# Kernel tuning notes

Measured on AMD Instinct MI355X. Metric: run time of the kernel, lower is better.

## Reference

```python
import jax, jax.numpy as jnp
import numpy as np

BN_EPS = 1e-5

def _batchnorm(x, gamma, beta):
    # torch BatchNorm1d in training mode: batch mean, biased variance
    mean = jnp.mean(x, axis=0)
    var = jnp.mean(jnp.square(x - mean), axis=0)
    return (x - mean) * jax.lax.rsqrt(var + BN_EPS) * gamma + beta

def setup_inputs() -> dict:
    key = jax.random.key(0)
    ks = jax.random.split(key, 6)
    N, E, D_atom, D_nbr = 50000, 1600000, 64, 64
    d_in, d_out = 2 * D_atom + D_nbr, 2 * D_atom  # 192, 128
    return {
        "atom_in_fea": jax.random.normal(ks[0], (N, D_atom), dtype=jnp.float32),
        "nbr_fea": jax.random.normal(ks[1], (E, D_nbr), dtype=jnp.float32),
        "edge_src": jax.random.randint(ks[2], (E,), 0, N),
        "edge_dst": jax.random.randint(ks[3], (E,), 0, N),
        "W": jax.random.normal(ks[4], (d_in, d_out), dtype=jnp.float32) * (1.0 / np.sqrt(d_in)),
        "b": jax.random.normal(ks[5], (d_out,), dtype=jnp.float32) * 0.01,
        "bn1_gamma": jnp.ones((d_out,), dtype=jnp.float32),
        "bn1_beta": jnp.zeros((d_out,), dtype=jnp.float32),
        "bn2_gamma": jnp.ones((D_atom,), dtype=jnp.float32),
        "bn2_beta": jnp.zeros((D_atom,), dtype=jnp.float32),
    }

def reference(atom_in_fea, nbr_fea, edge_src, edge_dst, W, b,
              bn1_gamma, bn1_beta, bn2_gamma, bn2_beta):
    N, D = atom_in_fea.shape
    # gather endpoints, concat with edge features: [E, 2D + D_nbr]
    total_fea = jnp.concatenate(
        [atom_in_fea[edge_src], atom_in_fea[edge_dst], nbr_fea], axis=1)
    total_fea = _batchnorm(total_fea @ W + b, bn1_gamma, bn1_beta)
    filter_fea, core_fea = jnp.split(total_fea, 2, axis=1)
    nbr_msg = jax.nn.sigmoid(filter_fea) * jax.nn.softplus(core_fea)  # [E, D]
    # scatter-add messages to destination atoms
    atom_update = jax.ops.segment_sum(nbr_msg, edge_dst, num_segments=N)
    atom_update = _batchnorm(atom_update, bn2_gamma, bn2_beta)
    return jax.nn.softplus(atom_in_fea + atom_update)
```

## Files before the change

### kernel.cpp

```cpp
#include <hip/hip_runtime.h>
#include <hip/hip_bf16.h>

typedef __attribute__((ext_vector_type(8))) short short8;
typedef __attribute__((ext_vector_type(4))) float floatx4;

__device__ __forceinline__ float bits2f(unsigned short u) {
    union { unsigned int i; float f; } v; v.i = ((unsigned int)u) << 16; return v.f;
}
__device__ __forceinline__ unsigned short f2bb(float x) {
    union { float f; unsigned int i; } v; v.f = x;
    unsigned int r = v.i + 0x7FFFu + ((v.i >> 16) & 1u);
    return (unsigned short)(r >> 16);
}
__device__ __forceinline__ float ldf(const void* base, long i, int fp32) {
    return fp32 ? ((const float*)base)[i] : bits2f(((const unsigned short*)base)[i]);
}
__device__ __forceinline__ short8 loadRow8(const void* base, long off, int fp32) {
    short8 r;
    if (!fp32) {
        r = *(const short8*)((const unsigned short*)base + off);
    } else {
        const float* f = (const float*)base + off;
        #pragma unroll
        for (int j = 0; j < 8; ++j) r[j] = (short)f2bb(f[j]);
    }
    return r;
}
__device__ __forceinline__ float lclamp(float z) {
    return fminf(fmaxf(z, -1e4f), 1e4f);
}

__global__ void k_probe(const unsigned short* __restrict__ Wb, int* __restrict__ flag) {
    int t = threadIdx.x;
    unsigned short u = Wb[t * 2];
    unsigned e = (u >> 7) & 0xFF;
    int in = (e >= 0x60 && e <= 0x8F) ? 1 : 0;
    unsigned long long m = __ballot(in);
    if (t == 0) flag[0] = (__popcll(m) < 32) ? 1 : 0;
}

__global__ __launch_bounds__(256) void k_atom_proj(
    const void* __restrict__ atom,
    const void* __restrict__ Wv,
    const void* __restrict__ bv,
    __hip_bfloat16* __restrict__ P, int N, const int* __restrict__ flagp)
{
    const int fp32 = *flagp;
    const int t = threadIdx.x;
    const int wave = t >> 6, lane = t & 63;
    const int half = wave & 1;
    const int pairInBlk = wave >> 1;
    const int n0 = lane & 15, kq = lane >> 4;

    short8 bf[8][2];
    #pragma unroll
    for (int tt = 0; tt < 8; ++tt)
        #pragma unroll
        for (int h = 0; h < 2; ++h)
            #pragma unroll
            for (int jj = 0; jj < 8; ++jj) {
                int k = half*64 + h*32 + kq*8 + jj;
                bf[tt][h][jj] = (short)f2bb(ldf(Wv, (long)k*128 + tt*16 + n0, fp32));
            }
    float bias[8];
    #pragma unroll
    for (int tt = 0; tt < 8; ++tt)
        bias[tt] = half ? 0.f : ldf(bv, tt*16 + n0, fp32);

    const long nGroups = ((long)N + 15) / 16;
    for (long g = (long)blockIdx.x*2 + pairInBlk; g < nGroups; g += (long)gridDim.x*2) {
        long a0 = g * 16;
        long am = a0 + n0;
        short8 a_lo = {}, a_hi = {};
        if (am < N) {
            a_lo = loadRow8(atom, am*64 + kq*8, fp32);
            a_hi = loadRow8(atom, am*64 + 32 + kq*8, fp32);
        }
        #pragma unroll
        for (int tt = 0; tt < 8; ++tt) {
            floatx4 c = {0.f, 0.f, 0.f, 0.f};
            c = __builtin_amdgcn_mfma_f32_16x16x32_bf16(a_lo, bf[tt][0], c, 0, 0, 0);
            c = __builtin_amdgcn_mfma_f32_16x16x32_bf16(a_hi, bf[tt][1], c, 0, 0, 0);
            #pragma unroll
            for (int r = 0; r < 4; ++r) {
                long a = a0 + kq*4 + r;
                if (a < N)
                    P[a*256 + half*128 + tt*16 + n0] =
                        __float2bfloat16(lclamp(c[r] + bias[tt]));
            }
        }
    }
}

template<int PHASE>
__global__ __launch_bounds__(256) void k_edge(
    const void* __restrict__ nbr,
    const int* __restrict__ esrc,
    const int* __restrict__ edst,
    const void* __restrict__ Wv,
    const unsigned short* __restrict__ Pb,
    const float* __restrict__ coef,
    float* __restrict__ outAcc,
    long E, const int* __restrict__ flagp)
{
    __shared__ float s_sum[128], s_ss[128];
    const int fp32 = *flagp;
    const int t = threadIdx.x;
    const int wave = t >> 6, lane = t & 63;
    const int n0 = lane & 15, kq = lane >> 4;

    short8 bf[8][2];
    #pragma unroll
    for (int tt = 0; tt < 8; ++tt)
        #pragma unroll
        for (int h = 0; h < 2; ++h)
            #pragma unroll
            for (int jj = 0; jj < 8; ++jj) {
                int k = 128 + h*32 + kq*8 + jj;
                bf[tt][h][jj] = (short)f2bb(ldf(Wv, (long)k*128 + tt*16 + n0, fp32));
            }

    float sc[8], sh[8];
    if (PHASE == 1) {
        #pragma unroll
        for (int tt = 0; tt < 8; ++tt) {
            sc[tt] = coef[tt*16 + n0];
            sh[tt] = coef[128 + tt*16 + n0];
        }
    }
    float lsum[8], lss[8];
    if (PHASE == 0) {
        if (t < 128) { s_sum[t] = 0.f; s_ss[t] = 0.f; }
        #pragma unroll
        for (int tt = 0; tt < 8; ++tt) { lsum[tt] = 0.f; lss[tt] = 0.f; }
    }

    const long nGroups = (E + 15) / 16;
    for (long g = (long)blockIdx.x*4 + wave; g < nGroups; g += (long)gridDim.x*4) {
        long e0 = g * 16;
        long ea = e0 + n0;
        short8 a_lo = {}, a_hi = {};
        if (ea < E) {
            a_lo = loadRow8(nbr, ea*64 + kq*8, fp32);
            a_hi = loadRow8(nbr, ea*64 + 32 + kq*8, fp32);
        }
        floatx4 acc[8];
        #pragma unroll
        for (int tt = 0; tt < 8; ++tt) {
            floatx4 c = {0.f, 0.f, 0.f, 0.f};
            c = __builtin_amdgcn_mfma_f32_16x16x32_bf16(a_lo, bf[tt][0], c, 0, 0, 0);
            c = __builtin_amdgcn_mfma_f32_16x16x32_bf16(a_hi, bf[tt][1], c, 0, 0, 0);
            acc[tt] = c;
        }
        int sE[4], dE[4];
        #pragma unroll
        for (int r = 0; r < 4; ++r) {
            long er = e0 + kq*4 + r;
            sE[r] = (er < E) ? esrc[er] : 0;
            dE[r] = (er < E) ? edst[er] : 0;
        }
        if (PHASE == 0) {
            #pragma unroll
            for (int tt = 0; tt < 8; ++tt) {
                int n = tt*16 + n0;
                #pragma unroll
                for (int r = 0; r < 4; ++r) {
                    long er = e0 + kq*4 + r;
                    if (er < E) {
                        float z = lclamp(acc[tt][r]
                                + bits2f(Pb[(long)sE[r]*256 + n])
                                + bits2f(Pb[(long)dE[r]*256 + 128 + n]));
                        lsum[tt] += z; lss[tt] += z*z;
                    }
                }
            }
        } else {
            float zh[8][4];
            #pragma unroll
            for (int tt = 0; tt < 8; ++tt) {
                int n = tt*16 + n0;
                #pragma unroll
                for (int r = 0; r < 4; ++r) {
                    float z = lclamp(acc[tt][r]
                            + bits2f(Pb[(long)sE[r]*256 + n])
                            + bits2f(Pb[(long)dE[r]*256 + 128 + n]));
                    zh[tt][r] = z * sc[tt] + sh[tt];
                }
            }
            #pragma unroll
            for (int tt = 0; tt < 4; ++tt) {
                #pragma unroll
                for (int r = 0; r < 4; ++r) {
                    long er = e0 + kq*4 + r;
                    if (er < E) {
                        float f = zh[tt][r], c = zh[tt+4][r];
                        float sig = 1.f / (1.f + __expf(-f));
                        float sp  = fmaxf(c, 0.f) + log1pf(__expf(-fabsf(c)));
                        atomicAdd(outAcc + (long)dE[r]*64 + tt*16 + n0, sig * sp);
                    }
                }
            }
        }
    }
    if (PHASE == 0) {
        __syncthreads();
        #pragma unroll
        for (int tt = 0; tt < 8; ++tt) {
            atomicAdd(&s_sum[tt*16 + n0], lsum[tt]);
            atomicAdd(&s_ss[tt*16 + n0], lss[tt]);
        }
        __syncthreads();
        if (t < 128) {
            atomicAdd(&outAcc[t], s_sum[t]);
            atomicAdd(&outAcc[128 + t], s_ss[t]);
        }
    }
}

__global__ void k_fin1(const float* __restrict__ stats,
                       const void* __restrict__ gamma,
                       const void* __restrict__ beta,
                       float* __restrict__ coef, float invE,
                       const int* __restrict__ flagp)
{
    const int fp32 = *flagp;
    int t = threadIdx.x;
    float mean = stats[t] * invE;
    float var  = fmaxf(stats[128 + t] * invE - mean * mean, 0.f);
    float sc = ldf(gamma, t, fp32) * rsqrtf(var + 1e-5f);
    coef[t] = sc;
    coef[128 + t] = ldf(beta, t, fp32) - mean * sc;
}

__global__ void k_au_stats(const float* __restrict__ au, float* __restrict__ stats, int N)
{
    __shared__ float s_red[256];
    int t = threadIdx.x;
    int j = t & 63, r = t >> 6;
    float lsum = 0.f, lss = 0.f;
    for (int base = blockIdx.x * 4; base < N; base += gridDim.x * 4) {
        int a = base + r;
        if (a < N) { float v = au[(long)a*64 + j]; lsum += v; lss += v*v; }
    }
    s_red[t] = lsum; __syncthreads();
    if (t < 64) atomicAdd(&stats[j], s_red[j] + s_red[j+64] + s_red[j+128] + s_red[j+192]);
    __syncthreads();
    s_red[t] = lss; __syncthreads();
    if (t < 64) atomicAdd(&stats[64+j], s_red[j] + s_red[j+64] + s_red[j+128] + s_red[j+192]);
}

__global__ void k_fin2(const float* __restrict__ stats,
                       const void* __restrict__ gamma,
                       const void* __restrict__ beta,
                       float* __restrict__ coef, float invN,
                       const int* __restrict__ flagp)
{
    const int fp32 = *flagp;
    int t = threadIdx.x;
    float mean = stats[t] * invN;
    float var  = fmaxf(stats[64 + t] * invN - mean * mean, 0.f);
    float sc = ldf(gamma, t, fp32) * rsqrtf(var + 1e-5f);
    coef[t] = sc;
    coef[64 + t] = ldf(beta, t, fp32) - mean * sc;
}

__global__ void k_out(const void* __restrict__ atom,
                      const float* __restrict__ au,
                      const float* __restrict__ coef2,
                      void* __restrict__ out, long total,
                      const int* __restrict__ flagp)
{
    const int fp32 = *flagp;
    long i = (long)blockIdx.x * blockDim.x + threadIdx.x;
    if (i >= total) return;
    int j = (int)(i & 63);
    float x = lclamp(ldf(atom, i, fp32) + au[i] * coef2[j] + coef2[64 + j]);
    float sp = fmaxf(x, 0.f) + log1pf(__expf(-fabsf(x)));
    if (fp32) ((float*)out)[i] = sp;
    else      ((__hip_bfloat16*)out)[i] = __float2bfloat16(sp);
}

extern "C" void kernel_launch(void* const* d_in, const int* in_sizes, int n_in,
                              void* d_out, int out_size, void* d_ws, size_t ws_size,
                              hipStream_t stream)
{
    const void* atom = d_in[0];
    const void* nbr  = d_in[1];
    const int* esrc = (const int*)d_in[2];
    const int* edst = (const int*)d_in[3];
    const void* Wv  = d_in[4];
    const void* bv  = d_in[5];
    const void* g1  = d_in[6];
    const void* be1 = d_in[7];
    const void* g2  = d_in[8];
    const void* be2 = d_in[9];

    const int  N = in_sizes[0] / 64;
    const long E = (long)in_sizes[1] / 64;

    char* w = (char*)d_ws;
    __hip_bfloat16* P = (__hip_bfloat16*)w;  w += (size_t)N * 256 * sizeof(__hip_bfloat16);
    float* au     = (float*)w;               w += (size_t)N * 64 * sizeof(float);
    float* stats1 = (float*)w;               w += 256 * sizeof(float);
    float* stats2 = (float*)w;               w += 128 * sizeof(float);
    float* coef1  = (float*)w;               w += 256 * sizeof(float);
    float* coef2  = (float*)w;               w += 128 * sizeof(float);
    int* flagp    = (int*)w;

    hipMemsetAsync(au, 0, (size_t)N * 64 * sizeof(float), stream);
    hipMemsetAsync(stats1, 0, 384 * sizeof(float), stream);

    k_probe<<<1, 64, 0, stream>>>((const unsigned short*)Wv, flagp);
    k_atom_proj<<<1024, 256, 0, stream>>>(atom, Wv, bv, P, N, flagp);
    k_edge<0><<<2048, 256, 0, stream>>>(nbr, esrc, edst, Wv,
                                        (const unsigned short*)P, nullptr, stats1, E, flagp);
    k_fin1<<<1, 128, 0, stream>>>(stats1, g1, be1, coef1, 1.0f / (float)E, flagp);
    k_edge<1><<<2048, 256, 0, stream>>>(nbr, esrc, edst, Wv,
                                        (const unsigned short*)P, coef1, au, E, flagp);
    k_au_stats<<<1024, 256, 0, stream>>>(au, stats2, N);
    k_fin2<<<1, 64, 0, stream>>>(stats2, g2, be2, coef2, 1.0f / (float)N, flagp);
    long total = (long)N * 64;
    k_out<<<(int)((total + 255) / 256), 256, 0, stream>>>(atom, au, coef2,
                                                          d_out, total, flagp);
}
```

Measured before the change: 1.716 ms.

## Materialize edge pre-activations in bf16 to avoid recomputing GEMM and gathers

```diff
diff --git a/kernel.cpp b/kernel.cpp
--- a/kernel.cpp
+++ b/kernel.cpp
@@ -3,6 +3,7 @@
 
 typedef __attribute__((ext_vector_type(8))) short short8;
 typedef __attribute__((ext_vector_type(4))) float floatx4;
+typedef __attribute__((ext_vector_type(4))) unsigned short us4;
 
 __device__ __forceinline__ float bits2f(unsigned short u) {
     union { unsigned int i; float f; } v; v.i = ((unsigned int)u) << 16; return v.f;
@@ -40,10 +41,9 @@
 }
 
 __global__ __launch_bounds__(256) void k_atom_proj(
-    const void* __restrict__ atom,
-    const void* __restrict__ Wv,
-    const void* __restrict__ bv,
-    __hip_bfloat16* __restrict__ P, int N, const int* __restrict__ flagp)
+    const void* __restrict__ atom, const void* __restrict__ Wv,
+    const void* __restrict__ bv, __hip_bfloat16* __restrict__ P,
+    int N, const int* __restrict__ flagp)
 {
     const int fp32 = *flagp;
     const int t = threadIdx.x;
@@ -92,15 +92,14 @@
     }
 }
 
-template<int PHASE>
-__global__ __launch_bounds__(256) void k_edge(
+__global__ __launch_bounds__(256) void k_edge_gemm(
     const void* __restrict__ nbr,
     const int* __restrict__ esrc,
     const int* __restrict__ edst,
     const void* __restrict__ Wv,
     const unsigned short* __restrict__ Pb,
-    const float* __restrict__ coef,
-    float* __restrict__ outAcc,
+    float* __restrict__ stats,
+    unsigned short* __restrict__ z,
     long E, const int* __restrict__ flagp)
 {
     __shared__ float s_sum[128], s_ss[128];
@@ -109,6 +108,141 @@
     const int wave = t >> 6, lane = t & 63;
     const int n0 = lane & 15, kq = lane >> 4;
 
+    if (t < 128) { s_sum[t] = 0.f; s_ss[t] = 0.f; }
+    __syncthreads();
+
+    short8 af[8][2];
+    #pragma unroll
+    for (int tt = 0; tt < 8; ++tt)
+        #pragma unroll
+        for (int h = 0; h < 2; ++h)
+            #pragma unroll
+            for (int jj = 0; jj < 8; ++jj) {
+                int k = 128 + h*32 + kq*8 + jj;
+                af[tt][h][jj] = (short)f2bb(ldf(Wv, (long)k*128 + tt*16 + n0, fp32));
+            }
+
+    float lsum[8][4], lss[8][4];
+    #pragma unroll
+    for (int tt = 0; tt < 8; ++tt)
+        #pragma unroll
+        for (int r = 0; r < 4; ++r) { lsum[tt][r] = 0.f; lss[tt][r] = 0.f; }
+
+    const long nG = (E + 15) / 16;
+    for (long g = (long)blockIdx.x*4 + wave; g < nG; g += (long)gridDim.x*4) {
+        long e0 = g * 16;
+        long e  = e0 + n0;
+        bool ev = (e < E);
+        short8 b_lo = {}, b_hi = {};
+        int sE = 0, dE = 0;
+        if (ev) {
+            b_lo = loadRow8(nbr, e*64 + kq*8, fp32);
+            b_hi = loadRow8(nbr, e*64 + 32 + kq*8, fp32);
+            sE = esrc[e]; dE = edst[e];
+        }
+        us4 p1[8], p2[8];
+        #pragma unroll
+        for (int tt = 0; tt < 8; ++tt) {
+            p1[tt] = *(const us4*)(Pb + (long)sE*256 + tt*16 + kq*4);
+            p2[tt] = *(const us4*)(Pb + (long)dE*256 + 128 + tt*16 + kq*4);
+        }
+        #pragma unroll
+        for (int tt = 0; tt < 8; ++tt) {
+            floatx4 c = {0.f, 0.f, 0.f, 0.f};
+            c = __builtin_amdgcn_mfma_f32_16x16x32_bf16(af[tt][0], b_lo, c, 0, 0, 0);
+            c = __builtin_amdgcn_mfma_f32_16x16x32_bf16(af[tt][1], b_hi, c, 0, 0, 0);
+            us4 zo;
+            #pragma unroll
+            for (int r = 0; r < 4; ++r) {
+                float zv = lclamp(c[r] + bits2f(p1[tt][r]) + bits2f(p2[tt][r]));
+                zo[r] = f2bb(zv);
+                if (ev) { lsum[tt][r] += zv; lss[tt][r] += zv*zv; }
+            }
+            if (ev) *(us4*)(z + e*128 + tt*16 + kq*4) = zo;
+        }
+    }
+    #pragma unroll
+    for (int tt = 0; tt < 8; ++tt)
+        #pragma unroll
+        for (int r = 0; r < 4; ++r) {
+            int n = tt*16 + kq*4 + r;
+            atomicAdd(&s_sum[n], lsum[tt][r]);
+            atomicAdd(&s_ss[n],  lss[tt][r]);
+        }
+    __syncthreads();
+    if (t < 128) {
+        atomicAdd(&stats[t], s_sum[t]);
+        atomicAdd(&stats[128 + t], s_ss[t]);
+    }
+}
+
+__global__ __launch_bounds__(256) void k_apply(
+    const unsigned short* __restrict__ z,
+    const int* __restrict__ edst,
+    const float* __restrict__ coef,
+    float* __restrict__ au, long E)
+{
+    const int t = threadIdx.x;
+    const int wave = t >> 6, lane = t & 63;
+    const int esub = lane >> 4, fg = lane & 15;
+
+    float sc[8], sh[8];
+    #pragma unroll
+    for (int j = 0; j < 8; ++j) {
+        sc[j] = coef[fg*8 + j];
+        sh[j] = coef[128 + fg*8 + j];
+    }
+
+    const long nG = (E + 3) / 4;
+    for (long g = (long)blockIdx.x*4 + wave; g < nG; g += (long)gridDim.x*4) {
+        long e = g*4 + esub;
+        bool ev = (e < E);
+        short8 zr = {};
+        int dE = 0;
+        if (ev) {
+            zr = *(const short8*)((const short*)z + e*128 + fg*8);
+            dE = edst[e];
+        }
+        float v[8];
+        #pragma unroll
+        for (int j = 0; j < 8; ++j)
+            v[j] = bits2f((unsigned short)zr[j]) * sc[j] + sh[j];
+        float p[8];
+        #pragma unroll
+        for (int j = 0; j < 8; ++j) p[j] = __shfl_xor(v[j], 8);
+        if (ev) {
+            if (fg < 8) {
+                #pragma unroll
+                for (int j = 0; j < 4; ++j) {
+                    float sig = 1.f / (1.f + __expf(-v[j]));
+                    float sp  = fmaxf(p[j], 0.f) + log1pf(__expf(-fabsf(p[j])));
+                    atomicAdd(au + (long)dE*64 + fg*8 + j, sig * sp);
+                }
+            } else {
+                #pragma unroll
+                for (int j = 4; j < 8; ++j) {
+                    float sig = 1.f / (1.f + __expf(-p[j]));
+                    float sp  = fmaxf(v[j], 0.f) + log1pf(__expf(-fabsf(v[j])));
+                    atomicAdd(au + (long)dE*64 + (fg - 8)*8 + j, sig * sp);
+                }
+            }
+        }
+    }
+}
+
+template<int PHASE>
+__global__ __launch_bounds__(256) void k_edge(
+    const void* __restrict__ nbr, const int* __restrict__ esrc,
+    const int* __restrict__ edst, const void* __restrict__ Wv,
+    const unsigned short* __restrict__ Pb, const float* __restrict__ coef,
+    float* __restrict__ outAcc, long E, const int* __restrict__ flagp)
+{
+    __shared__ float s_sum[128], s_ss[128];
+    const int fp32 = *flagp;
+    const int t = threadIdx.x;
+    const int wave = t >> 6, lane = t & 63;
+    const int n0 = lane & 15, kq = lane >> 4;
+
     short8 bf[8][2];
     #pragma unroll
     for (int tt = 0; tt < 8; ++tt)
@@ -119,7 +253,6 @@
                 int k = 128 + h*32 + kq*8 + jj;
                 bf[tt][h][jj] = (short)f2bb(ldf(Wv, (long)k*128 + tt*16 + n0, fp32));
             }
-
     float sc[8], sh[8];
     if (PHASE == 1) {
         #pragma unroll
@@ -133,8 +266,8 @@
         if (t < 128) { s_sum[t] = 0.f; s_ss[t] = 0.f; }
         #pragma unroll
         for (int tt = 0; tt < 8; ++tt) { lsum[tt] = 0.f; lss[tt] = 0.f; }
-    }
-
+        __syncthreads();
+    }
     const long nGroups = (E + 15) / 16;
     for (long g = (long)blockIdx.x*4 + wave; g < nGroups; g += (long)gridDim.x*4) {
         long e0 = g * 16;
@@ -167,10 +300,10 @@
                 for (int r = 0; r < 4; ++r) {
                     long er = e0 + kq*4 + r;
                     if (er < E) {
-                        float z = lclamp(acc[tt][r]
+                        float zv = lclamp(acc[tt][r]
                                 + bits2f(Pb[(long)sE[r]*256 + n])
                                 + bits2f(Pb[(long)dE[r]*256 + 128 + n]));
-                        lsum[tt] += z; lss[tt] += z*z;
+                        lsum[tt] += zv; lss[tt] += zv*zv;
                     }
                 }
             }
@@ -181,14 +314,14 @@
                 int n = tt*16 + n0;
                 #pragma unroll
                 for (int r = 0; r < 4; ++r) {
-                    float z = lclamp(acc[tt][r]
+                    float zv = lclamp(acc[tt][r]
                             + bits2f(Pb[(long)sE[r]*256 + n])
                             + bits2f(Pb[(long)dE[r]*256 + 128 + n]));
-                    zh[tt][r] = z * sc[tt] + sh[tt];
+                    zh[tt][r] = zv * sc[tt] + sh[tt];
                 }
             }
             #pragma unroll
-            for (int tt = 0; tt < 4; ++tt) {
+            for (int tt = 0; tt < 4; ++tt)
                 #pragma unroll
                 for (int r = 0; r < 4; ++r) {
                     long er = e0 + kq*4 + r;
@@ -199,11 +332,9 @@
                         atomicAdd(outAcc + (long)dE[r]*64 + tt*16 + n0, sig * sp);
                     }
                 }
-            }
         }
     }
     if (PHASE == 0) {
-        __syncthreads();
         #pragma unroll
         for (int tt = 0; tt < 8; ++tt) {
             atomicAdd(&s_sum[tt*16 + n0], lsum[tt]);
@@ -218,10 +349,8 @@
 }
 
 __global__ void k_fin1(const float* __restrict__ stats,
-                       const void* __restrict__ gamma,
-                       const void* __restrict__ beta,
-                       float* __restrict__ coef, float invE,
-                       const int* __restrict__ flagp)
+                       const void* __restrict__ gamma, const void* __restrict__ beta,
+                       float* __restrict__ coef, float invE, const int* __restrict__ flagp)
 {
     const int fp32 = *flagp;
     int t = threadIdx.x;
@@ -250,10 +379,8 @@
 }
 
 __global__ void k_fin2(const float* __restrict__ stats,
-                       const void* __restrict__ gamma,
-                       const void* __restrict__ beta,
-                       float* __restrict__ coef, float invN,
-                       const int* __restrict__ flagp)
+                       const void* __restrict__ gamma, const void* __restrict__ beta,
+                       float* __restrict__ coef, float invN, const int* __restrict__ flagp)
 {
     const int fp32 = *flagp;
     int t = threadIdx.x;
@@ -264,11 +391,9 @@
     coef[64 + t] = ldf(beta, t, fp32) - mean * sc;
 }
 
-__global__ void k_out(const void* __restrict__ atom,
-                      const float* __restrict__ au,
-                      const float* __restrict__ coef2,
-                      void* __restrict__ out, long total,
-                      const int* __restrict__ flagp)
+__global__ void k_out(const void* __restrict__ atom, const float* __restrict__ au,
+                      const float* __restrict__ coef2, void* __restrict__ out,
+                      long total, const int* __restrict__ flagp)
 {
     const int fp32 = *flagp;
     long i = (long)blockIdx.x * blockDim.x + threadIdx.x;
@@ -305,18 +430,30 @@
     float* stats2 = (float*)w;               w += 128 * sizeof(float);
     float* coef1  = (float*)w;               w += 256 * sizeof(float);
     float* coef2  = (float*)w;               w += 128 * sizeof(float);
-    int* flagp    = (int*)w;
+    int* flagp    = (int*)w;                 w += 256;
+    unsigned short* z = (unsigned short*)w;
+
+    const size_t fixed = (size_t)(w - (char*)d_ws);
+    const bool bigws = ws_size >= fixed + (size_t)E * 128 * sizeof(unsigned short);
 
     hipMemsetAsync(au, 0, (size_t)N * 64 * sizeof(float), stream);
     hipMemsetAsync(stats1, 0, 384 * sizeof(float), stream);
 
     k_probe<<<1, 64, 0, stream>>>((const unsigned short*)Wv, flagp);
     k_atom_proj<<<1024, 256, 0, stream>>>(atom, Wv, bv, P, N, flagp);
-    k_edge<0><<<2048, 256, 0, stream>>>(nbr, esrc, edst, Wv,
-                                        (const unsigned short*)P, nullptr, stats1, E, flagp);
-    k_fin1<<<1, 128, 0, stream>>>(stats1, g1, be1, coef1, 1.0f / (float)E, flagp);
-    k_edge<1><<<2048, 256, 0, stream>>>(nbr, esrc, edst, Wv,
-                                        (const unsigned short*)P, coef1, au, E, flagp);
+
+    if (bigws) {
+        k_edge_gemm<<<2048, 256, 0, stream>>>(nbr, esrc, edst, Wv,
+                                              (const unsigned short*)P, stats1, z, E, flagp);
+        k_fin1<<<1, 128, 0, stream>>>(stats1, g1, be1, coef1, 1.0f / (float)E, flagp);
+        k_apply<<<2048, 256, 0, stream>>>(z, edst, coef1, au, E);
+    } else {
+        k_edge<0><<<2048, 256, 0, stream>>>(nbr, esrc, edst, Wv,
+                                            (const unsigned short*)P, nullptr, stats1, E, flagp);
+        k_fin1<<<1, 128, 0, stream>>>(stats1, g1, be1, coef1, 1.0f / (float)E, flagp);
+        k_edge<1><<<2048, 256, 0, stream>>>(nbr, esrc, edst, Wv,
+                                            (const unsigned short*)P, coef1, au, E, flagp);
+    }
     k_au_stats<<<1024, 256, 0, stream>>>(au, stats2, N);
     k_fin2<<<1, 64, 0, stream>>>(stats2, g2, be2, coef2, 1.0f / (float)N, flagp);
     long total = (long)N * 64;
```

New measurement: 2.820 ms. 1.64x slower.
